# Optimization experiments

Hardware: AMD Instinct MI355X
Metric: run time of the kernel (lower is better)

The kernel has to match this reference:

```python
import jax, jax.numpy as jnp
import numpy as np

N_EMBD = 1024
D_K = 1024
D_V = 1024

def setup_inputs() -> dict:
    key = jax.random.key(0)
    k1, k2, k3, k4 = jax.random.split(key, 4)
    B, T = 4, 2048
    std = N_EMBD ** -0.5
    x = jax.random.normal(k1, (B, T, N_EMBD), dtype=jnp.float32)
    Wq = jax.random.normal(k2, (N_EMBD, D_K), dtype=jnp.float32) * std
    Wk = jax.random.normal(k3, (N_EMBD, D_K), dtype=jnp.float32) * std
    Wv = jax.random.normal(k4, (N_EMBD, D_V), dtype=jnp.float32) * std
    return {"x": x, "Wq": Wq, "Wk": Wk, "Wv": Wv}

def reference(x, Wq, Wk, Wv):
    # x: [B, T, C]
    T = x.shape[1]
    q = x @ Wq  # [B, T, d_k]
    k = x @ Wk  # [B, T, d_k]
    v = x @ Wv  # [B, T, d_v]
    scale = Wk.shape[1] ** -0.5
    wei = jnp.einsum('btd,bsd->bts', q, k) * scale  # [B, T, T]
    causal = jnp.tril(jnp.ones((T, T), dtype=bool))
    wei = jnp.where(causal, wei, -jnp.inf)
    wei = jax.nn.softmax(wei, axis=-1)
    return wei @ v  # [B, T, d_v]
```

## Files before the change

### kernel.cpp

```cpp
#include <hip/hip_runtime.h>
#include <hip/hip_bf16.h>
#include <stdint.h>

using bf16_t = __hip_bfloat16;
typedef __bf16 bf16x8 __attribute__((ext_vector_type(8)));
typedef float f32x4 __attribute__((ext_vector_type(4)));

__device__ __forceinline__ void async_lds16(const void* g, void* l) {
  __builtin_amdgcn_global_load_lds(
      (const __attribute__((address_space(1))) void*)g,
      (__attribute__((address_space(3))) void*)l, 16, 0, 0);
}

__device__ __forceinline__ unsigned short f2bf_u16(float f) {
  __hip_bfloat16 h = __float2bfloat16(f);
  return __builtin_bit_cast(unsigned short, h);
}

__global__ __launch_bounds__(256) void convert_x_kernel(
    const float* __restrict__ x, bf16_t* __restrict__ xb) {
  size_t i = ((size_t)blockIdx.x * 256 + threadIdx.x) * 4;
  float4 v = *(const float4*)(x + i);
  ushort4 o;
  o.x = f2bf_u16(v.x);
  o.y = f2bf_u16(v.y);
  o.z = f2bf_u16(v.z);
  o.w = f2bf_u16(v.w);
  *(ushort4*)(xb + i) = o;
}

__global__ __launch_bounds__(256) void convert_transpose_w_kernel(
    const float* __restrict__ Wq, const float* __restrict__ Wk,
    const float* __restrict__ Wv, bf16_t* __restrict__ wt) {
  __shared__ bf16_t tile[32][33];
  const float* W = (blockIdx.z == 0) ? Wq : (blockIdx.z == 1) ? Wk : Wv;
  bf16_t* WT = wt + (size_t)blockIdx.z * 1024 * 1024;
  const int tx = threadIdx.x & 31;
  const int ty = threadIdx.x >> 5;
  const int bx = blockIdx.x & 31;
  const int by = blockIdx.x >> 5;
  const int k0 = by * 32, n0 = bx * 32;
#pragma unroll
  for (int j = 0; j < 32; j += 8)
    tile[ty + j][tx] = __float2bfloat16(W[(size_t)(k0 + ty + j) * 1024 + n0 + tx]);
  __syncthreads();
#pragma unroll
  for (int j = 0; j < 32; j += 8)
    WT[(size_t)(n0 + ty + j) * 1024 + k0 + tx] = tile[tx][ty + j];
}

template <int OUT_MODE, bool CAUSAL_SKIP, bool KLIMIT>
__global__ __launch_bounds__(256) void gemm_bt_kernel(
    const bf16_t* __restrict__ A, const bf16_t* __restrict__ BT,
    void* __restrict__ Cv, void* __restrict__ Cv2, void* __restrict__ Cv3,
    int M, int N, int K, int lda, int ldb, int ldc,
    long long aBatch, long long bBatch, long long cBatch) {
  const int m0 = blockIdx.y * 128;
  const int n0 = blockIdx.x * 128;
  if (CAUSAL_SKIP && n0 > m0) return;
  A += (size_t)blockIdx.z * aBatch;
  BT += (size_t)blockIdx.z * bBatch;
  int nkt = K >> 5;
  if (KLIMIT) {
    int lim = (m0 + 128) >> 5;
    nkt = nkt < lim ? nkt : lim;
  }

  __shared__ bf16_t lsA[128 * 32];
  __shared__ bf16_t lsB[128 * 32];

  const int tid = threadIdx.x;
  const int wid = tid >> 6;
  const int lane = tid & 63;
  const int wr = wid >> 1;
  const int wc = wid & 1;

  f32x4 acc[4][4];
  const f32x4 zero = {0.f, 0.f, 0.f, 0.f};
#pragma unroll
  for (int m = 0; m < 4; ++m)
#pragma unroll
    for (int n = 0; n < 4; ++n) acc[m][n] = zero;

  const int srow = tid >> 2;
  const int scol = (tid & 3) * 8;
  const bf16_t* gA = A + (size_t)(m0 + srow) * lda + scol;
  const bf16_t* gB = BT + (size_t)(n0 + srow) * ldb + scol;
  const size_t gAstep64 = (size_t)64 * lda;
  const size_t gBstep64 = (size_t)64 * ldb;

  bf16_t* lA0 = lsA + wid * 512;
  bf16_t* lA1 = lsA + 2048 + wid * 512;
  bf16_t* lB0 = lsB + wid * 512;
  bf16_t* lB1 = lsB + 2048 + wid * 512;

  const int frow = lane & 15;
  const int fk = (lane >> 4) * 8;
  const int aoff = (wr * 64 + frow) * 32 + fk;
  const int boff = (wc * 64 + frow) * 32 + fk;

  for (int kt = 0; kt < nkt; ++kt) {
    __syncthreads();
    async_lds16(gA, lA0);
    async_lds16(gA + gAstep64, lA1);
    async_lds16(gB, lB0);
    async_lds16(gB + gBstep64, lB1);
    gA += 32;
    gB += 32;
    __syncthreads();

    bf16x8 af[4], bfr[4];
#pragma unroll
    for (int m = 0; m < 4; ++m)
      af[m] = *(const bf16x8*)(lsA + aoff + m * 16 * 32);
#pragma unroll
    for (int n = 0; n < 4; ++n)
      bfr[n] = *(const bf16x8*)(lsB + boff + n * 16 * 32);
#pragma unroll
    for (int m = 0; m < 4; ++m)
#pragma unroll
      for (int n = 0; n < 4; ++n)
        acc[m][n] =
            __builtin_amdgcn_mfma_f32_16x16x32_bf16(af[m], bfr[n], acc[m][n], 0, 0, 0);
  }

  const int erow = wr * 64 + (lane >> 4) * 4;
  const int ecol = wc * 64 + (lane & 15);
  if (OUT_MODE == 2) {
    float* C = (float*)Cv + (size_t)blockIdx.z * cBatch;
#pragma unroll
    for (int m = 0; m < 4; ++m)
#pragma unroll
      for (int n = 0; n < 4; ++n)
#pragma unroll
        for (int j = 0; j < 4; ++j) {
          int r = m0 + erow + m * 16 + j;
          int c = n0 + ecol + n * 16;
          C[(size_t)r * ldc + c] = acc[m][n][j];
        }
  } else {
    if (n0 < 2048) {
      bf16_t* C = (bf16_t*)((n0 < 1024) ? Cv : Cv2);
      const int cbase = (n0 < 1024) ? 0 : 1024;
#pragma unroll
      for (int m = 0; m < 4; ++m)
#pragma unroll
        for (int n = 0; n < 4; ++n)
#pragma unroll
          for (int j = 0; j < 4; ++j) {
            int r = m0 + erow + m * 16 + j;
            int c = n0 + ecol + n * 16 - cbase;
            C[(size_t)r * 1024 + c] = __float2bfloat16(acc[m][n][j]);
          }
    } else {
      bf16_t* C = (bf16_t*)Cv3;
#pragma unroll
      for (int m = 0; m < 4; ++m)
#pragma unroll
        for (int n = 0; n < 4; ++n)
#pragma unroll
          for (int j = 0; j < 4; ++j) {
            int r = m0 + erow + m * 16 + j;
            int c = n0 + ecol + n * 16 - 2048;
            int b = r >> 11, t = r & 2047;
            C[((size_t)b * 1024 + c) * 2048 + t] = __float2bfloat16(acc[m][n][j]);
          }
    }
  }
}

__global__ __launch_bounds__(256) void softmax_causal_kernel(float* __restrict__ S) {
  const int lane = threadIdx.x & 63;
  const int rg = blockIdx.x * 4 + (threadIdx.x >> 6);
  const int b = rg >> 11;
  const int t = rg & 2047;
  float* srow = S + (size_t)b * 2048 * 2048 + (size_t)t * 2048;

  float4 v[8];
#pragma unroll
  for (int it = 0; it < 8; ++it) v[it] = *(const float4*)(srow + (it * 64 + lane) * 4);

  float mx = -3.0e38f;
#pragma unroll
  for (int it = 0; it < 8; ++it) {
    int s0 = (it * 64 + lane) * 4;
    if (s0 + 0 <= t) mx = fmaxf(mx, v[it].x);
    if (s0 + 1 <= t) mx = fmaxf(mx, v[it].y);
    if (s0 + 2 <= t) mx = fmaxf(mx, v[it].z);
    if (s0 + 3 <= t) mx = fmaxf(mx, v[it].w);
  }
#pragma unroll
  for (int off = 32; off > 0; off >>= 1) mx = fmaxf(mx, __shfl_xor(mx, off, 64));

  const float kMul = 0.03125f * 1.4426950408889634f;
  float p[8][4];
  float sum = 0.f;
#pragma unroll
  for (int it = 0; it < 8; ++it) {
    int s0 = (it * 64 + lane) * 4;
    float e0 = (s0 + 0 <= t) ? exp2f((v[it].x - mx) * kMul) : 0.f;
    float e1 = (s0 + 1 <= t) ? exp2f((v[it].y - mx) * kMul) : 0.f;
    float e2 = (s0 + 2 <= t) ? exp2f((v[it].z - mx) * kMul) : 0.f;
    float e3 = (s0 + 3 <= t) ? exp2f((v[it].w - mx) * kMul) : 0.f;
    p[it][0] = e0; p[it][1] = e1; p[it][2] = e2; p[it][3] = e3;
    sum += (e0 + e1) + (e2 + e3);
  }
#pragma unroll
  for (int off = 32; off > 0; off >>= 1) sum += __shfl_xor(sum, off, 64);
  const float inv = 1.f / sum;

  bf16_t* prow = (bf16_t*)srow;
#pragma unroll
  for (int it = 0; it < 8; ++it) {
    ushort4 o;
    o.x = f2bf_u16(p[it][0] * inv);
    o.y = f2bf_u16(p[it][1] * inv);
    o.z = f2bf_u16(p[it][2] * inv);
    o.w = f2bf_u16(p[it][3] * inv);
    *(ushort4*)(prow + (it * 64 + lane) * 4) = o;
  }
}

extern "C" void kernel_launch(void* const* d_in, const int* in_sizes, int n_in,
                              void* d_out, int out_size, void* d_ws, size_t ws_size,
                              hipStream_t stream) {
  (void)in_sizes; (void)n_in; (void)out_size;
  const float* x = (const float*)d_in[0];
  const float* Wq = (const float*)d_in[1];
  const float* Wk = (const float*)d_in[2];
  const float* Wv = (const float*)d_in[3];
  float* out = (float*)d_out;

  char* ws = (char*)d_ws;
  const size_t NEED = 123731968;
  const bool batched = ws_size >= NEED;

  bf16_t* xb = (bf16_t*)ws;
  float* S;
  bf16_t *WT, *Qb, *Kb, *VT;
  if (batched) {
    S = (float*)ws;
    WT = (bf16_t*)(ws + 67108864);
    Qb = (bf16_t*)(ws + 73400320);
    Kb = (bf16_t*)(ws + 90177536);
    VT = (bf16_t*)(ws + 106954752);
  } else {
    S = (float*)ws;
    WT = (bf16_t*)(ws + 16777216);
    Qb = (bf16_t*)(ws + 16777216 + 6291456);
    Kb = Qb + 8388608;
    VT = Kb + 8388608;
  }

  convert_x_kernel<<<8192, 256, 0, stream>>>(x, xb);
  convert_transpose_w_kernel<<<dim3(1024, 1, 3), 256, 0, stream>>>(Wq, Wk, Wv, WT);

  gemm_bt_kernel<3, false, false><<<dim3(24, 64, 1), 256, 0, stream>>>(
      xb, WT, Qb, Kb, VT, 8192, 3072, 1024, 1024, 1024, 0, 0, 0, 0);

  if (batched) {
    gemm_bt_kernel<2, true, false><<<dim3(16, 16, 4), 256, 0, stream>>>(
        Qb, Kb, S, nullptr, nullptr, 2048, 2048, 1024, 1024, 1024, 2048,
        2097152LL, 2097152LL, 4194304LL);
    softmax_causal_kernel<<<2048, 256, 0, stream>>>(S);
    gemm_bt_kernel<2, false, true><<<dim3(8, 16, 4), 256, 0, stream>>>(
        (const bf16_t*)S, VT, out, nullptr, nullptr, 2048, 1024, 2048, 4096,
        2048, 1024, 8388608LL, 2097152LL, 2097152LL);
  } else {
    for (int b = 0; b < 4; ++b) {
      const size_t qoff = (size_t)b * 2048 * 1024;
      gemm_bt_kernel<2, true, false><<<dim3(16, 16, 1), 256, 0, stream>>>(
          Qb + qoff, Kb + qoff, S, nullptr, nullptr, 2048, 2048, 1024, 1024,
          1024, 2048, 0, 0, 0);
      softmax_causal_kernel<<<512, 256, 0, stream>>>(S);
      gemm_bt_kernel<2, false, true><<<dim3(8, 16, 1), 256, 0, stream>>>(
          (const bf16_t*)S, VT + qoff, out + qoff, nullptr, nullptr, 2048,
          1024, 2048, 4096, 2048, 1024, 0, 0, 0);
    }
  }
}
```

Before: 208.8 us.

## Replace GEMM with triple-buffered 128x256 pipelined kernel with LDS and XCD swizzles

Replaces the simple double-sync GEMM with a 512-thread kernel using 128x256 tiles. It triple-buffers async global-to-LDS loads, prefetching two K-steps ahead with explicit vmcnt waits, and splits the MFMA work into two halves around barriers with s_setprio. It also XOR-swizzles the LDS layout to reduce bank conflicts and remaps workgroups across XCDs for the projection GEMM. The aim is to hide memory latency and raise MFMA utilisation. The cost is higher LDS use and coarser causal tiles that compute some extra masked work.

```diff
diff --git a/kernel.cpp b/kernel.cpp
--- a/kernel.cpp
+++ b/kernel.cpp
@@ -49,15 +49,25 @@
     WT[(size_t)(n0 + ty + j) * 1024 + k0 + tx] = tile[tx][ty + j];
 }
 
-template <int OUT_MODE, bool CAUSAL_SKIP, bool KLIMIT>
-__global__ __launch_bounds__(256) void gemm_bt_kernel(
+template <int OUT_MODE, bool CAUSAL_SKIP, bool KLIMIT, bool XCDSWZ>
+__global__ __launch_bounds__(512, 2) void gemm_pipe_kernel(
     const bf16_t* __restrict__ A, const bf16_t* __restrict__ BT,
     void* __restrict__ Cv, void* __restrict__ Cv2, void* __restrict__ Cv3,
     int M, int N, int K, int lda, int ldb, int ldc,
     long long aBatch, long long bBatch, long long cBatch) {
-  const int m0 = blockIdx.y * 128;
-  const int n0 = blockIdx.x * 128;
-  if (CAUSAL_SKIP && n0 > m0) return;
+  int bx = blockIdx.x, by = blockIdx.y;
+  if (XCDSWZ) {
+    const int gx = gridDim.x;
+    const int nwg = gx * gridDim.y;
+    const int id = by * gx + bx;
+    const int cpx = nwg >> 3;
+    const int swz = (id & 7) * cpx + (id >> 3);
+    by = swz / gx;
+    bx = swz % gx;
+  }
+  const int m0 = by * 128;
+  const int n0 = bx * 256;
+  if (CAUSAL_SKIP && 2 * bx > by) return;
   A += (size_t)blockIdx.z * aBatch;
   BT += (size_t)blockIdx.z * bBatch;
   int nkt = K >> 5;
@@ -66,14 +76,25 @@
     nkt = nkt < lim ? nkt : lim;
   }
 
-  __shared__ bf16_t lsA[128 * 32];
-  __shared__ bf16_t lsB[128 * 32];
+  __shared__ bf16_t lsA[3 * 128 * 32];
+  __shared__ bf16_t lsB[3 * 256 * 32];
 
   const int tid = threadIdx.x;
   const int wid = tid >> 6;
   const int lane = tid & 63;
-  const int wr = wid >> 1;
-  const int wc = wid & 1;
+  const int wm = wid >> 2;
+  const int wn = wid & 3;
+
+  const int sr = tid >> 2;
+  const int ss = tid & 3;
+  const int sswz = ss ^ ((sr >> 1) & 3);
+  const bf16_t* gA = A + (size_t)(m0 + sr) * lda + sswz * 8;
+  const bf16_t* gB0 = BT + (size_t)(n0 + sr) * ldb + sswz * 8;
+  const bf16_t* gB1 = BT + (size_t)(n0 + 128 + sr) * ldb + sswz * 8;
+
+  const int kslot = (lane >> 4) ^ ((lane >> 1) & 3);
+  const int abase = (wm * 64 + (lane & 15)) * 32 + kslot * 8;
+  const int bbase = (wn * 64 + (lane & 15)) * 32 + kslot * 8;
 
   f32x4 acc[4][4];
   const f32x4 zero = {0.f, 0.f, 0.f, 0.f};
@@ -82,50 +103,73 @@
 #pragma unroll
     for (int n = 0; n < 4; ++n) acc[m][n] = zero;
 
-  const int srow = tid >> 2;
-  const int scol = (tid & 3) * 8;
-  const bf16_t* gA = A + (size_t)(m0 + srow) * lda + scol;
-  const bf16_t* gB = BT + (size_t)(n0 + srow) * ldb + scol;
-  const size_t gAstep64 = (size_t)64 * lda;
-  const size_t gBstep64 = (size_t)64 * ldb;
-
-  bf16_t* lA0 = lsA + wid * 512;
-  bf16_t* lA1 = lsA + 2048 + wid * 512;
-  bf16_t* lB0 = lsB + wid * 512;
-  bf16_t* lB1 = lsB + 2048 + wid * 512;
-
-  const int frow = lane & 15;
-  const int fk = (lane >> 4) * 8;
-  const int aoff = (wr * 64 + frow) * 32 + fk;
-  const int boff = (wc * 64 + frow) * 32 + fk;
-
-  for (int kt = 0; kt < nkt; ++kt) {
-    __syncthreads();
-    async_lds16(gA, lA0);
-    async_lds16(gA + gAstep64, lA1);
-    async_lds16(gB, lB0);
-    async_lds16(gB + gBstep64, lB1);
-    gA += 32;
-    gB += 32;
-    __syncthreads();
+  async_lds16(gA, lsA + wid * 512);
+  async_lds16(gB0, lsB + wid * 512);
+  async_lds16(gB1, lsB + 4096 + wid * 512);
+  if (nkt > 1) {
+    async_lds16(gA + 32, lsA + 4096 + wid * 512);
+    async_lds16(gB0 + 32, lsB + 8192 + wid * 512);
+    async_lds16(gB1 + 32, lsB + 8192 + 4096 + wid * 512);
+    asm volatile("s_waitcnt vmcnt(3)" ::: "memory");
+  } else {
+    asm volatile("s_waitcnt vmcnt(0)" ::: "memory");
+  }
+  __builtin_amdgcn_s_barrier();
+
+  int cb = 0;
+  for (int t = 0; t < nkt; ++t) {
+    const bf16_t* bufA = lsA + cb * 4096;
+    const bf16_t* bufB = lsB + cb * 8192;
+    int sb = cb + 2;
+    if (sb >= 3) sb -= 3;
 
     bf16x8 af[4], bfr[4];
 #pragma unroll
-    for (int m = 0; m < 4; ++m)
-      af[m] = *(const bf16x8*)(lsA + aoff + m * 16 * 32);
-#pragma unroll
-    for (int n = 0; n < 4; ++n)
-      bfr[n] = *(const bf16x8*)(lsB + boff + n * 16 * 32);
-#pragma unroll
-    for (int m = 0; m < 4; ++m)
-#pragma unroll
-      for (int n = 0; n < 4; ++n)
-        acc[m][n] =
-            __builtin_amdgcn_mfma_f32_16x16x32_bf16(af[m], bfr[n], acc[m][n], 0, 0, 0);
-  }
-
-  const int erow = wr * 64 + (lane >> 4) * 4;
-  const int ecol = wc * 64 + (lane & 15);
+    for (int mf = 0; mf < 4; ++mf)
+      af[mf] = *(const bf16x8*)(bufA + abase + mf * 512);
+    bfr[0] = *(const bf16x8*)(bufB + bbase);
+    bfr[1] = *(const bf16x8*)(bufB + bbase + 512);
+    if (t + 2 < nkt) {
+      async_lds16(gA + (t + 2) * 32, lsA + sb * 4096 + wid * 512);
+      async_lds16(gB0 + (t + 2) * 32, lsB + sb * 8192 + wid * 512);
+    }
+    __builtin_amdgcn_s_barrier();
+    __builtin_amdgcn_s_setprio(1);
+#pragma unroll
+    for (int mf = 0; mf < 4; ++mf)
+#pragma unroll
+      for (int nf = 0; nf < 2; ++nf)
+        acc[mf][nf] = __builtin_amdgcn_mfma_f32_16x16x32_bf16(
+            af[mf], bfr[nf], acc[mf][nf], 0, 0, 0);
+    __builtin_amdgcn_s_setprio(0);
+    __builtin_amdgcn_s_barrier();
+
+    bfr[2] = *(const bf16x8*)(bufB + bbase + 1024);
+    bfr[3] = *(const bf16x8*)(bufB + bbase + 1536);
+    if (t + 2 < nkt)
+      async_lds16(gB1 + (t + 2) * 32, lsB + sb * 8192 + 4096 + wid * 512);
+    if (t + 2 < nkt) {
+      asm volatile("s_waitcnt vmcnt(3)" ::: "memory");
+    } else if (t + 2 == nkt) {
+      asm volatile("s_waitcnt vmcnt(0)" ::: "memory");
+    }
+    __builtin_amdgcn_s_barrier();
+    __builtin_amdgcn_s_setprio(1);
+#pragma unroll
+    for (int mf = 0; mf < 4; ++mf)
+#pragma unroll
+      for (int nf = 2; nf < 4; ++nf)
+        acc[mf][nf] = __builtin_amdgcn_mfma_f32_16x16x32_bf16(
+            af[mf], bfr[nf], acc[mf][nf], 0, 0, 0);
+    __builtin_amdgcn_s_setprio(0);
+    __builtin_amdgcn_s_barrier();
+
+    cb = cb + 1;
+    if (cb >= 3) cb -= 3;
+  }
+
+  const int erow = wm * 64 + (lane >> 4) * 4;
+  const int ecol = wn * 64 + (lane & 15);
   if (OUT_MODE == 2) {
     float* C = (float*)Cv + (size_t)blockIdx.z * cBatch;
 #pragma unroll
@@ -141,7 +185,7 @@
   } else {
     if (n0 < 2048) {
       bf16_t* C = (bf16_t*)((n0 < 1024) ? Cv : Cv2);
-      const int cbase = (n0 < 1024) ? 0 : 1024;
+      const int cb0 = n0 & 1023;
 #pragma unroll
       for (int m = 0; m < 4; ++m)
 #pragma unroll
@@ -149,11 +193,12 @@
 #pragma unroll
           for (int j = 0; j < 4; ++j) {
             int r = m0 + erow + m * 16 + j;
-            int c = n0 + ecol + n * 16 - cbase;
+            int c = cb0 + ecol + n * 16;
             C[(size_t)r * 1024 + c] = __float2bfloat16(acc[m][n][j]);
           }
     } else {
       bf16_t* C = (bf16_t*)Cv3;
+      const int d0 = n0 - 2048;
 #pragma unroll
       for (int m = 0; m < 4; ++m)
 #pragma unroll
@@ -161,9 +206,9 @@
 #pragma unroll
           for (int j = 0; j < 4; ++j) {
             int r = m0 + erow + m * 16 + j;
-            int c = n0 + ecol + n * 16 - 2048;
-            int b = r >> 11, t = r & 2047;
-            C[((size_t)b * 1024 + c) * 2048 + t] = __float2bfloat16(acc[m][n][j]);
+            int d = d0 + ecol + n * 16;
+            int b = r >> 11, tt = r & 2047;
+            C[((size_t)b * 1024 + d) * 2048 + tt] = __float2bfloat16(acc[m][n][j]);
           }
     }
   }
@@ -255,25 +300,25 @@
   convert_x_kernel<<<8192, 256, 0, stream>>>(x, xb);
   convert_transpose_w_kernel<<<dim3(1024, 1, 3), 256, 0, stream>>>(Wq, Wk, Wv, WT);
 
-  gemm_bt_kernel<3, false, false><<<dim3(24, 64, 1), 256, 0, stream>>>(
+  gemm_pipe_kernel<3, false, false, true><<<dim3(12, 64, 1), 512, 0, stream>>>(
       xb, WT, Qb, Kb, VT, 8192, 3072, 1024, 1024, 1024, 0, 0, 0, 0);
 
   if (batched) {
-    gemm_bt_kernel<2, true, false><<<dim3(16, 16, 4), 256, 0, stream>>>(
+    gemm_pipe_kernel<2, true, false, false><<<dim3(8, 16, 4), 512, 0, stream>>>(
         Qb, Kb, S, nullptr, nullptr, 2048, 2048, 1024, 1024, 1024, 2048,
         2097152LL, 2097152LL, 4194304LL);
     softmax_causal_kernel<<<2048, 256, 0, stream>>>(S);
-    gemm_bt_kernel<2, false, true><<<dim3(8, 16, 4), 256, 0, stream>>>(
+    gemm_pipe_kernel<2, false, true, false><<<dim3(4, 16, 4), 512, 0, stream>>>(
         (const bf16_t*)S, VT, out, nullptr, nullptr, 2048, 1024, 2048, 4096,
         2048, 1024, 8388608LL, 2097152LL, 2097152LL);
   } else {
     for (int b = 0; b < 4; ++b) {
       const size_t qoff = (size_t)b * 2048 * 1024;
-      gemm_bt_kernel<2, true, false><<<dim3(16, 16, 1), 256, 0, stream>>>(
+      gemm_pipe_kernel<2, true, false, false><<<dim3(8, 16, 1), 512, 0, stream>>>(
           Qb + qoff, Kb + qoff, S, nullptr, nullptr, 2048, 2048, 1024, 1024,
           1024, 2048, 0, 0, 0);
       softmax_causal_kernel<<<512, 256, 0, stream>>>(S);
-      gemm_bt_kernel<2, false, true><<<dim3(8, 16, 1), 256, 0, stream>>>(
+      gemm_pipe_kernel<2, false, true, false><<<dim3(4, 16, 1), 512, 0, stream>>>(
           (const bf16_t*)S, VT + qoff, out + qoff, nullptr, nullptr, 2048,
           1024, 2048, 4096, 2048, 1024, 0, 0, 0);
     }
```

Result: faster. 187.0 us (-10.5%).
